# Kernel optimization log

Hardware: AMD Instinct MI355X
Metric: run time of the kernel (lower is better)

## Reference

```python
import jax, jax.numpy as jnp
import numpy as np

N0, N1, N2 = 20000, 15000, 15000
N = N0 + N1 + N2            # total nodes
E = 800000                  # edges (avg degree 16)
H, C = 128, 64


def setup_inputs() -> dict:
    key = jax.random.key(0)
    ks = jax.random.split(key, 16)
    s = 0.05  # weight scale
    return {
        "feat0": jax.random.normal(ks[0], (N0, 512), jnp.float32),
        "feat1": jax.random.normal(ks[1], (N1, 256), jnp.float32),
        "feat2": jax.random.normal(ks[2], (N2, 128), jnp.float32),
        "W0": jax.random.normal(ks[3], (512, H), jnp.float32) * s,
        "b0": jnp.zeros((H,), jnp.float32),
        "W1": jax.random.normal(ks[4], (256, H), jnp.float32) * s,
        "b1": jnp.zeros((H,), jnp.float32),
        "W2": jax.random.normal(ks[5], (128, H), jnp.float32) * s,
        "b2": jnp.zeros((H,), jnp.float32),
        "bias_l0": jnp.zeros((H,), jnp.float32),
        "W_l1": jax.random.normal(ks[6], (H, H), jnp.float32) * s,
        "b_l1": jnp.zeros((H,), jnp.float32),
        "W_l2": jax.random.normal(ks[7], (H, C), jnp.float32) * s,
        "b_l2": jnp.zeros((C,), jnp.float32),
        "src": jax.random.randint(ks[8], (E,), 0, N, jnp.int32),
        "dst": jax.random.randint(ks[9], (E,), 0, N, jnp.int32),
    }


def _norms(src, dst):
    # DGL GraphConv norm='both': src side uses out-degree, dst side in-degree
    ones = jnp.ones((E,), jnp.float32)
    deg_out = jax.ops.segment_sum(ones, src, num_segments=N)
    deg_in = jax.ops.segment_sum(ones, dst, num_segments=N)
    return jnp.maximum(deg_out, 1.0) ** -0.5, jnp.maximum(deg_in, 1.0) ** -0.5


def _agg(h, src, dst, norm_src, norm_dst):
    # normalized sparse aggregation: D_in^{-1/2} A D_out^{-1/2} h
    m = (h * norm_src[:, None])[src]                     # [E, d] gather
    a = jax.ops.segment_sum(m, dst, num_segments=N)      # [N, d] scatter-add
    return a * norm_dst[:, None]


def reference(feat0, feat1, feat2, W0, b0, W1, b1, W2, b2,
              bias_l0, W_l1, b_l1, W_l2, b_l2, src, dst):
    # per-node-type linear projections, concatenated along node axis
    h = jnp.concatenate([feat0 @ W0 + b0,
                         feat1 @ W1 + b1,
                         feat2 @ W2 + b2], axis=0)       # [N, H]
    ns, nd = _norms(src, dst)
    # layer 0: GraphConv(weight=False) -> agg + bias + relu (dropout = eval identity)
    h = jax.nn.relu(_agg(h, src, dst, ns, nd) + bias_l0)
    # layer 1: agg + linear + relu
    h = jax.nn.relu(_agg(h, src, dst, ns, nd) @ W_l1 + b_l1)
    # layer 2: agg + linear (no activation)
    h = _agg(h, src, dst, ns, nd) @ W_l2 + b_l2          # [N, C]
    return h
```

## Files before the change

### kernel.cpp

```cpp
#include <hip/hip_runtime.h>
#include <hip/hip_fp16.h>

#define N_NODES 50000
#define N0_ 20000
#define N1_ 15000
#define N2_ 15000
#define E_EDGES 800000
#define H_ 128
#define C_ 64

#define PB0 ((N0_ + 63) / 64)
#define PB1 ((N1_ + 63) / 64)
#define PB2 ((N2_ + 63) / 64)
#define PB_TOTAL (PB0 + PB1 + PB2)
#define EB ((E_EDGES + 255) / 256)
#define SB ((N_NODES + 255) / 256)

__device__ __forceinline__ float4 load_a4(const float* A, size_t idx) {
    return *reinterpret_cast<const float4*>(&A[idx]);
}
__device__ __forceinline__ float4 load_a4(const __half* A, size_t idx) {
    __half2 p0 = *reinterpret_cast<const __half2*>(&A[idx]);
    __half2 p1 = *reinterpret_cast<const __half2*>(&A[idx + 2]);
    float2 f0 = __half22float2(p0), f1 = __half22float2(p1);
    return make_float4(f0.x, f0.y, f1.x, f1.y);
}


template <int TN, bool BIAS, bool RELU, bool SCALE, typename IT, typename OT>
__device__ __forceinline__ void gemm_block(
    const IT* __restrict__ A, const float* __restrict__ W,
    const float* __restrict__ bias, const float* __restrict__ rowscale,
    OT* __restrict__ out, int M, int K, int m0, float* As, float* Bs) {
    constexpr int NJ = TN / 32;
    constexpr int TN4 = TN / 4;
    int tid = threadIdx.x;
    int tx = tid & 31;
    int ty = tid >> 5;

    float acc[8][NJ];
#pragma unroll
    for (int i = 0; i < 8; i++)
#pragma unroll
        for (int j = 0; j < NJ; j++) acc[i][j] = 0.f;

    for (int k0 = 0; k0 < K; k0 += 32) {
#pragma unroll
        for (int t0 = 0; t0 < 2; t0++) {
            int t = tid + t0 * 256;
            int row = t >> 3;
            int c = t & 7;
            float4 v = make_float4(0.f, 0.f, 0.f, 0.f);
            if (m0 + row < M) v = load_a4(A, (size_t)(m0 + row) * K + k0 + c * 4);
            As[(c * 4 + 0) * 68 + row] = v.x;
            As[(c * 4 + 1) * 68 + row] = v.y;
            As[(c * 4 + 2) * 68 + row] = v.z;
            As[(c * 4 + 3) * 68 + row] = v.w;
        }
#pragma unroll
        for (int t0 = 0; t0 < 32 * TN4 / 256; t0++) {
            int t = tid + t0 * 256;
            int r = t / TN4;
            int c4 = t % TN4;
            *reinterpret_cast<float4*>(&Bs[r * TN + c4 * 4]) =
                *reinterpret_cast<const float4*>(&W[(size_t)(k0 + r) * TN + c4 * 4]);
        }
        __syncthreads();
#pragma unroll 8
        for (int k = 0; k < 32; k++) {
            float4 a0 = *reinterpret_cast<float4*>(&As[k * 68 + ty * 8]);
            float4 a1 = *reinterpret_cast<float4*>(&As[k * 68 + ty * 8 + 4]);
            float ar[8] = {a0.x, a0.y, a0.z, a0.w, a1.x, a1.y, a1.z, a1.w};
            float br[NJ];
#pragma unroll
            for (int j = 0; j < NJ; j++) br[j] = Bs[k * TN + tx + 32 * j];
#pragma unroll
            for (int i = 0; i < 8; i++)
#pragma unroll
                for (int j = 0; j < NJ; j++) acc[i][j] = fmaf(ar[i], br[j], acc[i][j]);
        }
        __syncthreads();
    }
#pragma unroll
    for (int i = 0; i < 8; i++) {
        int row = m0 + ty * 8 + i;
        if (row < M) {
            float sc = SCALE ? rowscale[row] : 1.f;
#pragma unroll
            for (int j = 0; j < NJ; j++) {
                float v = acc[i][j] + (BIAS ? bias[tx + 32 * j] : 0.f);
                if (RELU) v = fmaxf(v, 0.f);
                v *= sc;
                out[(size_t)row * TN + tx + 32 * j] = (OT)v;
            }
        }
    }
}


__global__ __launch_bounds__(256) void k1_proj_rank(
    const float* __restrict__ feat0, const float* __restrict__ feat1, const float* __restrict__ feat2,
    const float* __restrict__ W0, const float* __restrict__ b0,
    const float* __restrict__ W1, const float* __restrict__ b1,
    const float* __restrict__ W2, const float* __restrict__ b2,
    __half* __restrict__ h0h,
    const int* __restrict__ src, const int* __restrict__ dst,
    int* __restrict__ cnt, int* __restrict__ degO, int* __restrict__ rank) {
    __shared__ float As[32 * 68];
    __shared__ float Bs[32 * 128];
    int bid = blockIdx.x;
    if (bid < PB_TOTAL) {
        const float* A; const float* Wp; const float* bp; __half* op; int M, K, m0;
        if (bid < PB0) {
            A = feat0; Wp = W0; bp = b0; op = h0h; M = N0_; K = 512; m0 = bid * 64;
        } else if (bid < PB0 + PB1) {
            A = feat1; Wp = W1; bp = b1; op = h0h + (size_t)N0_ * H_; M = N1_; K = 256;
            m0 = (bid - PB0) * 64;
        } else {
            A = feat2; Wp = W2; bp = b2; op = h0h + (size_t)(N0_ + N1_) * H_; M = N2_; K = 128;
            m0 = (bid - PB0 - PB1) * 64;
        }
        gemm_block<128, true, false, false, float, __half>(A, Wp, bp, nullptr, op, M, K, m0, As, Bs);
    } else {
        int e = (bid - PB_TOTAL) * 256 + threadIdx.x;
        if (e < E_EDGES) {
            rank[e] = atomicAdd(&cnt[dst[e]], 1);
            atomicAdd(&degO[src[e]], 1);
        }
    }
}


__global__ __launch_bounds__(256) void scan1_kernel(
    const int* __restrict__ cnt, int* __restrict__ pre, int* __restrict__ blocksum) {
    __shared__ int buf[256];
    int t = threadIdx.x;
    int i = blockIdx.x * 256 + t;
    int tot = (i < N_NODES) ? cnt[i] : 0;
    buf[t] = tot;
    __syncthreads();
#pragma unroll
    for (int off = 1; off < 256; off <<= 1) {
        int v = (t >= off) ? buf[t - off] : 0;
        __syncthreads();
        buf[t] += v;
        __syncthreads();
    }
    if (i < N_NODES) pre[i] = buf[t] - tot;
    if (t == 255) blocksum[blockIdx.x] = buf[255];
}

__global__ __launch_bounds__(256) void scan2_kernel(
    const int* __restrict__ blocksum, int* __restrict__ blockoff, int* __restrict__ rowptr) {
    __shared__ int buf[256];
    int t = threadIdx.x;
    int v = (t < SB) ? blocksum[t] : 0;
    buf[t] = v;
    __syncthreads();
#pragma unroll
    for (int off = 1; off < 256; off <<= 1) {
        int u = (t >= off) ? buf[t - off] : 0;
        __syncthreads();
        buf[t] += u;
        __syncthreads();
    }
    if (t < SB) blockoff[t] = buf[t] - v;
    if (t == 255) rowptr[N_NODES] = buf[255];
}

__global__ __launch_bounds__(256) void scan3_fill_kernel(
    const int* __restrict__ cnt, const int* __restrict__ degO, const int* __restrict__ pre,
    const int* __restrict__ blockoff, int* __restrict__ rowptr,
    float* __restrict__ ns, float* __restrict__ nd,
    const int* __restrict__ src, const int* __restrict__ dst,
    const int* __restrict__ rank, int* __restrict__ col) {
    int bid = blockIdx.x;
    if (bid < SB) {
        int i = bid * 256 + threadIdx.x;
        if (i < N_NODES) {
            rowptr[i] = blockoff[bid] + pre[i];
            ns[i] = rsqrtf(fmaxf((float)degO[i], 1.0f));
            nd[i] = rsqrtf(fmaxf((float)cnt[i], 1.0f));
        }
    } else {
        int e = (bid - SB) * 256 + threadIdx.x;
        if (e < E_EDGES) {
            int d = dst[e];
            int rp = blockoff[d >> 8] + pre[d];
            col[rp + rank[e]] = src[e];
        }
    }
}


template <int CH, int NSLOAD, int EPI, int OUTH, int DEPTH>
__global__ __launch_bounds__(256) void agg_h_kernel(
    const __half* __restrict__ h, const int* __restrict__ rowptr,
    const int* __restrict__ col, const float* __restrict__ ns,
    const float* __restrict__ nd, const float* __restrict__ bias,
    void* __restrict__ out) {
    constexpr int L = CH / 8;
    constexpr int EPW = 64 / L;
    int node = blockIdx.x * 4 + (threadIdx.x >> 6);
    if (node >= N_NODES) return;
    int lane = threadIdx.x & 63;
    int li = lane & (L - 1);
    int g = lane / L;
    const uint4* __restrict__ h8 = (const uint4*)h;
    int beg = rowptr[node], end = rowptr[node + 1];
    float acc[DEPTH][8];
#pragma unroll
    for (int d = 0; d < DEPTH; d++)
#pragma unroll
        for (int j = 0; j < 8; j++) acc[d][j] = 0.f;
    union U8 { uint4 u; __half2 h2[4]; };
    int e = beg + g;
    for (; e + (DEPTH - 1) * EPW < end; e += DEPTH * EPW) {
        int s[DEPTH];
        U8 u[DEPTH];
        float w[DEPTH];
#pragma unroll
        for (int d = 0; d < DEPTH; d++) s[d] = col[e + d * EPW];
#pragma unroll
        for (int d = 0; d < DEPTH; d++) {
            u[d].u = h8[(size_t)s[d] * L + li];
            w[d] = NSLOAD ? ns[s[d]] : 1.f;
        }
#pragma unroll
        for (int d = 0; d < DEPTH; d++)
#pragma unroll
            for (int p = 0; p < 4; p++) {
                float2 f = __half22float2(u[d].h2[p]);
                if (NSLOAD) {
                    acc[d][2 * p] = fmaf(w[d], f.x, acc[d][2 * p]);
                    acc[d][2 * p + 1] = fmaf(w[d], f.y, acc[d][2 * p + 1]);
                } else {
                    acc[d][2 * p] += f.x;
                    acc[d][2 * p + 1] += f.y;
                }
            }
    }
    for (; e < end; e += EPW) {
        int s = col[e];
        U8 u0;
        u0.u = h8[(size_t)s * L + li];
        float w0 = NSLOAD ? ns[s] : 1.f;
#pragma unroll
        for (int p = 0; p < 4; p++) {
            float2 f = __half22float2(u0.h2[p]);
            if (NSLOAD) {
                acc[0][2 * p] = fmaf(w0, f.x, acc[0][2 * p]);
                acc[0][2 * p + 1] = fmaf(w0, f.y, acc[0][2 * p + 1]);
            } else {
                acc[0][2 * p] += f.x;
                acc[0][2 * p + 1] += f.y;
            }
        }
    }
    float a0[8];
#pragma unroll
    for (int j = 0; j < 8; j++) {
        float v = acc[0][j];
#pragma unroll
        for (int d = 1; d < DEPTH; d++) v += acc[d][j];
#pragma unroll
        for (int off = 32; off >= L; off >>= 1) v += __shfl_xor(v, off);
        a0[j] = v;
    }
    if (lane < L) {
        float w = nd[node];
#pragma unroll
        for (int j = 0; j < 8; j++) a0[j] *= w;
        if (EPI == 1) {
            float sc = ns[node];
#pragma unroll
            for (int j = 0; j < 8; j++)
                a0[j] = fmaxf(a0[j] + bias[li * 8 + j], 0.f) * sc;
        } else if (EPI == 2) {
#pragma unroll
            for (int j = 0; j < 8; j++) a0[j] += bias[li * 8 + j];
        }
        if (OUTH) {
            union { uint4 u; __half hh[8]; } cv;
#pragma unroll
            for (int j = 0; j < 8; j++) cv.hh[j] = __float2half(a0[j]);
            ((uint4*)out)[(size_t)node * L + li] = cv.u;
        } else {
            float4* o4 = (float4*)out;
            o4[(size_t)node * (CH / 4) + li * 2] = make_float4(a0[0], a0[1], a0[2], a0[3]);
            o4[(size_t)node * (CH / 4) + li * 2 + 1] = make_float4(a0[4], a0[5], a0[6], a0[7]);
        }
    }
}


template <int TN, bool BIAS, bool RELU, bool SCALE, typename IT, typename OT>
__global__ __launch_bounds__(256) void gemm_kernel(
    const IT* __restrict__ A, const float* __restrict__ W,
    const float* __restrict__ bias, const float* __restrict__ rowscale,
    OT* __restrict__ out, int M, int K) {
    __shared__ float As[32 * 68];
    __shared__ float Bs[32 * TN];
    gemm_block<TN, BIAS, RELU, SCALE, IT, OT>(A, W, bias, rowscale, out, M, K, blockIdx.x * 64, As, Bs);
}


extern "C" void kernel_launch(void* const* d_in, const int* in_sizes, int n_in,
                              void* d_out, int out_size, void* d_ws, size_t ws_size,
                              hipStream_t stream) {
    const float* feat0 = (const float*)d_in[0];
    const float* feat1 = (const float*)d_in[1];
    const float* feat2 = (const float*)d_in[2];
    const float* W0 = (const float*)d_in[3];
    const float* b0 = (const float*)d_in[4];
    const float* W1 = (const float*)d_in[5];
    const float* b1 = (const float*)d_in[6];
    const float* W2 = (const float*)d_in[7];
    const float* b2 = (const float*)d_in[8];
    const float* bias_l0 = (const float*)d_in[9];
    const float* W_l1 = (const float*)d_in[10];
    const float* b_l1 = (const float*)d_in[11];
    const float* W_l2 = (const float*)d_in[12];
    const float* b_l2 = (const float*)d_in[13];
    const int* src = (const int*)d_in[14];
    const int* dst = (const int*)d_in[15];
    float* out = (float*)d_out;

    char* ws = (char*)d_ws;
    size_t off = 0;
    auto alloc = [&](size_t bytes) {
        size_t cur = off;
        off += (bytes + 255) & ~(size_t)255;
        return cur;
    };
    size_t h0h_off = alloc((size_t)N_NODES * H_ * 2);
    size_t h1h_off = alloc((size_t)N_NODES * H_ * 2);
    size_t hAh_off = alloc((size_t)N_NODES * H_ * 2);
    size_t hBh_off = alloc((size_t)N_NODES * H_ * 2);
    size_t h2h_off = alloc((size_t)N_NODES * C_ * 2);
    size_t cnt_off = alloc((size_t)N_NODES * 4);
    size_t degO_off = alloc((size_t)N_NODES * 4);
    size_t ns_off = alloc((size_t)N_NODES * 4);
    size_t nd_off = alloc((size_t)N_NODES * 4);
    size_t rowptr_off = alloc((size_t)(N_NODES + 1) * 4);
    size_t rank_off = alloc((size_t)E_EDGES * 4);
    size_t col_off = alloc((size_t)E_EDGES * 4);
    size_t pre_off = alloc((size_t)N_NODES * 4);
    size_t bsum_off = alloc((size_t)SB * 4);
    size_t boff_off = alloc((size_t)SB * 4);

    __half* h0h = (__half*)(ws + h0h_off);
    __half* h1h = (__half*)(ws + h1h_off);
    __half* hAh = (__half*)(ws + hAh_off);
    __half* hBh = (__half*)(ws + hBh_off);
    __half* h2h = (__half*)(ws + h2h_off);
    int* cnt = (int*)(ws + cnt_off);
    int* degO = (int*)(ws + degO_off);
    float* ns = (float*)(ws + ns_off);
    float* nd = (float*)(ws + nd_off);
    int* rowptr = (int*)(ws + rowptr_off);
    int* rank = (int*)(ws + rank_off);
    int* col = (int*)(ws + col_off);
    int* pre = (int*)(ws + pre_off);
    int* bsum = (int*)(ws + bsum_off);
    int* boff = (int*)(ws + boff_off);

    hipMemsetAsync(ws + cnt_off, 0, ns_off - cnt_off, stream);

    k1_proj_rank<<<PB_TOTAL + EB, 256, 0, stream>>>(
        feat0, feat1, feat2, W0, b0, W1, b1, W2, b2, h0h, src, dst, cnt, degO, rank);
    scan1_kernel<<<SB, 256, 0, stream>>>(cnt, pre, bsum);
    scan2_kernel<<<1, 256, 0, stream>>>(bsum, boff, rowptr);
    scan3_fill_kernel<<<SB + EB, 256, 0, stream>>>(
        cnt, degO, pre, boff, rowptr, ns, nd, src, dst, rank, col);

    const int AGB = (N_NODES + 3) / 4;
    agg_h_kernel<128, 1, 1, 1, 4><<<AGB, 256, 0, stream>>>(h0h, rowptr, col, ns, nd, bias_l0, h1h);
    agg_h_kernel<128, 0, 0, 1, 4><<<AGB, 256, 0, stream>>>(h1h, rowptr, col, ns, nd, nullptr, hAh);
    gemm_kernel<128, true, true, true, __half, __half><<<(N_NODES + 63) / 64, 256, 0, stream>>>(
        hAh, W_l1, b_l1, ns, hBh, N_NODES, 128);
    gemm_kernel<64, false, false, false, __half, __half><<<(N_NODES + 63) / 64, 256, 0, stream>>>(
        hBh, W_l2, nullptr, nullptr, h2h, N_NODES, 128);
    agg_h_kernel<64, 0, 2, 0, 2><<<AGB, 256, 0, stream>>>(h2h, rowptr, col, ns, nd, b_l2, out);
}
```

Before: 272.0 us.

## Use split-fp16 MFMA for input projection GEMM and simplify aggregation unroll

Replaces the scalar FP32 tiled GEMM for the per-type input projections with MFMA 16x16x32 f16 instructions. Inputs and weights are split into hi/lo fp16 parts and combined with three MFMAs to keep roughly fp32 accuracy. The aggregation kernel also drops its templated depth and always uses a fixed 2-way edge unroll, which lowers memory-level parallelism for layers that previously used depth 4. The split conversion adds extra LDS traffic and conversion work, and the transposed B stores into shared memory may cause bank conflicts.

```diff
diff --git a/kernel.cpp b/kernel.cpp
--- a/kernel.cpp
+++ b/kernel.cpp
@@ -15,6 +15,10 @@
 #define PB_TOTAL (PB0 + PB1 + PB2)
 #define EB ((E_EDGES + 255) / 256)
 #define SB ((N_NODES + 255) / 256)
+
+typedef _Float16 half4_t __attribute__((ext_vector_type(4)));
+typedef _Float16 half8_t __attribute__((ext_vector_type(8)));
+typedef float f32x4 __attribute__((ext_vector_type(4)));
 
 __device__ __forceinline__ float4 load_a4(const float* A, size_t idx) {
     return *reinterpret_cast<const float4*>(&A[idx]);
@@ -106,23 +110,92 @@
     __half* __restrict__ h0h,
     const int* __restrict__ src, const int* __restrict__ dst,
     int* __restrict__ cnt, int* __restrict__ degO, int* __restrict__ rank) {
-    __shared__ float As[32 * 68];
-    __shared__ float Bs[32 * 128];
+    __shared__ _Float16 smem[15360];
     int bid = blockIdx.x;
+    int tid = threadIdx.x;
     if (bid < PB_TOTAL) {
-        const float* A; const float* Wp; const float* bp; __half* op; int M, K, m0;
+        const float* A; const float* Wp; const float* bp; int M, K, m0;
         if (bid < PB0) {
-            A = feat0; Wp = W0; bp = b0; op = h0h; M = N0_; K = 512; m0 = bid * 64;
+            A = feat0; Wp = W0; bp = b0; M = N0_; K = 512; m0 = bid * 64;
         } else if (bid < PB0 + PB1) {
-            A = feat1; Wp = W1; bp = b1; op = h0h + (size_t)N0_ * H_; M = N1_; K = 256;
-            m0 = (bid - PB0) * 64;
+            A = feat1; Wp = W1; bp = b1; M = N1_; K = 256; m0 = (bid - PB0) * 64;
         } else {
-            A = feat2; Wp = W2; bp = b2; op = h0h + (size_t)(N0_ + N1_) * H_; M = N2_; K = 128;
-            m0 = (bid - PB0 - PB1) * 64;
-        }
-        gemm_block<128, true, false, false, float, __half>(A, Wp, bp, nullptr, op, M, K, m0, As, Bs);
+            A = feat2; Wp = W2; bp = b2; M = N2_; K = 128; m0 = (bid - PB0 - PB1) * 64;
+        }
+        size_t obase = (bid < PB0) ? 0 : ((bid < PB0 + PB1) ? (size_t)N0_ * H_
+                                                            : (size_t)(N0_ + N1_) * H_);
+        _Float16* Ah = smem;
+        _Float16* Al = smem + 2560;
+        _Float16* Bh = smem + 5120;
+        _Float16* Bl = smem + 10240;
+
+        int wv = tid >> 6;
+        int lane = tid & 63;
+        int lm = lane & 15;
+        int ks = lane >> 4;
+
+        f32x4 acc[8];
+#pragma unroll
+        for (int j = 0; j < 8; j++)
+#pragma unroll
+            for (int r = 0; r < 4; r++) acc[j][r] = 0.f;
+
+        for (int k0 = 0; k0 < K; k0 += 32) {
+#pragma unroll
+            for (int t0 = 0; t0 < 2; t0++) {
+                int idx = tid + t0 * 256;
+                int row = idx >> 3;
+                int c = idx & 7;
+                float4 v = make_float4(0.f, 0.f, 0.f, 0.f);
+                if (m0 + row < M)
+                    v = *reinterpret_cast<const float4*>(&A[(size_t)(m0 + row) * K + k0 + c * 4]);
+                _Float16 hx = (_Float16)v.x, hy = (_Float16)v.y;
+                _Float16 hz = (_Float16)v.z, hw = (_Float16)v.w;
+                half4_t hi = {hx, hy, hz, hw};
+                half4_t lo = {(_Float16)(v.x - (float)hx), (_Float16)(v.y - (float)hy),
+                              (_Float16)(v.z - (float)hz), (_Float16)(v.w - (float)hw)};
+                *reinterpret_cast<half4_t*>(&Ah[row * 40 + c * 4]) = hi;
+                *reinterpret_cast<half4_t*>(&Al[row * 40 + c * 4]) = lo;
+            }
+#pragma unroll
+            for (int t0 = 0; t0 < 4; t0++) {
+                int idx = tid + t0 * 256;
+                int kr = idx >> 5;
+                int c4 = idx & 31;
+                float4 v = *reinterpret_cast<const float4*>(&Wp[(size_t)(k0 + kr) * 128 + c4 * 4]);
+                float f[4] = {v.x, v.y, v.z, v.w};
+#pragma unroll
+                for (int j = 0; j < 4; j++) {
+                    _Float16 hi = (_Float16)f[j];
+                    Bh[(c4 * 4 + j) * 40 + kr] = hi;
+                    Bl[(c4 * 4 + j) * 40 + kr] = (_Float16)(f[j] - (float)hi);
+                }
+            }
+            __syncthreads();
+            half8_t ah = *reinterpret_cast<half8_t*>(&Ah[(16 * wv + lm) * 40 + ks * 8]);
+            half8_t al = *reinterpret_cast<half8_t*>(&Al[(16 * wv + lm) * 40 + ks * 8]);
+#pragma unroll
+            for (int j = 0; j < 8; j++) {
+                half8_t bh = *reinterpret_cast<half8_t*>(&Bh[(16 * j + lm) * 40 + ks * 8]);
+                half8_t bl = *reinterpret_cast<half8_t*>(&Bl[(16 * j + lm) * 40 + ks * 8]);
+                acc[j] = __builtin_amdgcn_mfma_f32_16x16x32_f16(ah, bh, acc[j], 0, 0, 0);
+                acc[j] = __builtin_amdgcn_mfma_f32_16x16x32_f16(al, bh, acc[j], 0, 0, 0);
+                acc[j] = __builtin_amdgcn_mfma_f32_16x16x32_f16(ah, bl, acc[j], 0, 0, 0);
+            }
+            __syncthreads();
+        }
+#pragma unroll
+        for (int j = 0; j < 8; j++) {
+            int colg = 16 * j + lm;
+            float bb = bp[colg];
+#pragma unroll
+            for (int r = 0; r < 4; r++) {
+                int row = m0 + 16 * wv + ks * 4 + r;
+                if (row < M) h0h[obase + (size_t)row * H_ + colg] = (__half)(acc[j][r] + bb);
+            }
+        }
     } else {
-        int e = (bid - PB_TOTAL) * 256 + threadIdx.x;
+        int e = (bid - PB_TOTAL) * 256 + tid;
         if (e < E_EDGES) {
             rank[e] = atomicAdd(&cnt[dst[e]], 1);
             atomicAdd(&degO[src[e]], 1);
@@ -193,7 +266,7 @@
 }
 
 
-template <int CH, int NSLOAD, int EPI, int OUTH, int DEPTH>
+template <int CH, int NSLOAD, int EPI, int OUTH>
 __global__ __launch_bounds__(256) void agg_h_kernel(
     const __half* __restrict__ h, const int* __restrict__ rowptr,
     const int* __restrict__ col, const float* __restrict__ ns,
@@ -208,61 +281,54 @@
     int g = lane / L;
     const uint4* __restrict__ h8 = (const uint4*)h;
     int beg = rowptr[node], end = rowptr[node + 1];
-    float acc[DEPTH][8];
-#pragma unroll
-    for (int d = 0; d < DEPTH; d++)
-#pragma unroll
-        for (int j = 0; j < 8; j++) acc[d][j] = 0.f;
+    float a0[8] = {0.f, 0.f, 0.f, 0.f, 0.f, 0.f, 0.f, 0.f};
+    float a1[8] = {0.f, 0.f, 0.f, 0.f, 0.f, 0.f, 0.f, 0.f};
     union U8 { uint4 u; __half2 h2[4]; };
     int e = beg + g;
-    for (; e + (DEPTH - 1) * EPW < end; e += DEPTH * EPW) {
-        int s[DEPTH];
-        U8 u[DEPTH];
-        float w[DEPTH];
-#pragma unroll
-        for (int d = 0; d < DEPTH; d++) s[d] = col[e + d * EPW];
-#pragma unroll
-        for (int d = 0; d < DEPTH; d++) {
-            u[d].u = h8[(size_t)s[d] * L + li];
-            w[d] = NSLOAD ? ns[s[d]] : 1.f;
-        }
-#pragma unroll
-        for (int d = 0; d < DEPTH; d++)
-#pragma unroll
-            for (int p = 0; p < 4; p++) {
-                float2 f = __half22float2(u[d].h2[p]);
-                if (NSLOAD) {
-                    acc[d][2 * p] = fmaf(w[d], f.x, acc[d][2 * p]);
-                    acc[d][2 * p + 1] = fmaf(w[d], f.y, acc[d][2 * p + 1]);
-                } else {
-                    acc[d][2 * p] += f.x;
-                    acc[d][2 * p + 1] += f.y;
-                }
-            }
-    }
-    for (; e < end; e += EPW) {
+    for (; e + EPW < end; e += 2 * EPW) {
+        int s0 = col[e], s1 = col[e + EPW];
+        U8 u0, u1;
+        u0.u = h8[(size_t)s0 * L + li];
+        u1.u = h8[(size_t)s1 * L + li];
+        float w0 = NSLOAD ? ns[s0] : 1.f;
+        float w1 = NSLOAD ? ns[s1] : 1.f;
+#pragma unroll
+        for (int p = 0; p < 4; p++) {
+            float2 f0 = __half22float2(u0.h2[p]);
+            float2 f1 = __half22float2(u1.h2[p]);
+            if (NSLOAD) {
+                a0[2 * p] = fmaf(w0, f0.x, a0[2 * p]);
+                a0[2 * p + 1] = fmaf(w0, f0.y, a0[2 * p + 1]);
+                a1[2 * p] = fmaf(w1, f1.x, a1[2 * p]);
+                a1[2 * p + 1] = fmaf(w1, f1.y, a1[2 * p + 1]);
+            } else {
+                a0[2 * p] += f0.x;
+                a0[2 * p + 1] += f0.y;
+                a1[2 * p] += f1.x;
+                a1[2 * p + 1] += f1.y;
+            }
+        }
+    }
+    if (e < end) {
         int s = col[e];
         U8 u0;
         u0.u = h8[(size_t)s * L + li];
         float w0 = NSLOAD ? ns[s] : 1.f;
 #pragma unroll
         for (int p = 0; p < 4; p++) {
-            float2 f = __half22float2(u0.h2[p]);
+            float2 f0 = __half22float2(u0.h2[p]);
             if (NSLOAD) {
-                acc[0][2 * p] = fmaf(w0, f.x, acc[0][2 * p]);
-                acc[0][2 * p + 1] = fmaf(w0, f.y, acc[0][2 * p + 1]);
+                a0[2 * p] = fmaf(w0, f0.x, a0[2 * p]);
+                a0[2 * p + 1] = fmaf(w0, f0.y, a0[2 * p + 1]);
             } else {
-                acc[0][2 * p] += f.x;
-                acc[0][2 * p + 1] += f.y;
-            }
-        }
-    }
-    float a0[8];
+                a0[2 * p] += f0.x;
+                a0[2 * p + 1] += f0.y;
+            }
+        }
+    }
 #pragma unroll
     for (int j = 0; j < 8; j++) {
-        float v = acc[0][j];
-#pragma unroll
-        for (int d = 1; d < DEPTH; d++) v += acc[d][j];
+        float v = a0[j] + a1[j];
 #pragma unroll
         for (int off = 32; off >= L; off >>= 1) v += __shfl_xor(v, off);
         a0[j] = v;
@@ -375,11 +441,11 @@
         cnt, degO, pre, boff, rowptr, ns, nd, src, dst, rank, col);
 
     const int AGB = (N_NODES + 3) / 4;
-    agg_h_kernel<128, 1, 1, 1, 4><<<AGB, 256, 0, stream>>>(h0h, rowptr, col, ns, nd, bias_l0, h1h);
-    agg_h_kernel<128, 0, 0, 1, 4><<<AGB, 256, 0, stream>>>(h1h, rowptr, col, ns, nd, nullptr, hAh);
+    agg_h_kernel<128, 1, 1, 1><<<AGB, 256, 0, stream>>>(h0h, rowptr, col, ns, nd, bias_l0, h1h);
+    agg_h_kernel<128, 0, 0, 1><<<AGB, 256, 0, stream>>>(h1h, rowptr, col, ns, nd, nullptr, hAh);
     gemm_kernel<128, true, true, true, __half, __half><<<(N_NODES + 63) / 64, 256, 0, stream>>>(
         hAh, W_l1, b_l1, ns, hBh, N_NODES, 128);
     gemm_kernel<64, false, false, false, __half, __half><<<(N_NODES + 63) / 64, 256, 0, stream>>>(
         hBh, W_l2, nullptr, nullptr, h2h, N_NODES, 128);
-    agg_h_kernel<64, 0, 2, 0, 2><<<AGB, 256, 0, stream>>>(h2h, rowptr, col, ns, nd, b_l2, out);
-}
+    agg_h_kernel<64, 0, 2, 0><<<AGB, 256, 0, stream>>>(h2h, rowptr, col, ns, nd, b_l2, out);
+}
```

Result: slower. 308.1 us (+13.3%).
